# Optimization experiments

Hardware: AMD Instinct MI355X
Metric: run time of the kernel (lower is better)

## Reference

```python
import jax, jax.numpy as jnp
import numpy as np

H = 128          # input hidden dim
HID = 128        # expert hidden width
OUT = 128        # out_channels
NR = 8           # n_routed
NS = 2           # n_shared
RDIM = 16        # router feature dim


def setup_inputs() -> dict:
    key = jax.random.key(0)
    ks = jax.random.split(key, 11)
    s = 0.05
    x = jax.random.normal(ks[0], (2, 32, 32, 32, H), dtype=jnp.float32)
    # router params
    Wr1 = jax.random.normal(ks[1], (H, RDIM), dtype=jnp.float32) * s
    br1 = jnp.zeros((RDIM,), dtype=jnp.float32)
    Wr2 = jax.random.normal(ks[2], (RDIM, NR), dtype=jnp.float32) * s
    br2 = jnp.zeros((NR,), dtype=jnp.float32)
    # routed expert params, stacked on leading expert axis
    We1 = jax.random.normal(ks[3], (NR, H, HID), dtype=jnp.float32) * s
    be1 = jnp.zeros((NR, HID), dtype=jnp.float32)
    We2 = jax.random.normal(ks[4], (NR, HID, OUT), dtype=jnp.float32) * s
    be2 = jnp.zeros((NR, OUT), dtype=jnp.float32)
    # shared expert params
    Ws1 = jax.random.normal(ks[5], (NS, H, HID), dtype=jnp.float32) * s
    bs1 = jnp.zeros((NS, HID), dtype=jnp.float32)
    Ws2 = jax.random.normal(ks[6], (NS, HID, OUT), dtype=jnp.float32) * s
    bs2 = jnp.zeros((NS, OUT), dtype=jnp.float32)
    return dict(x=x, Wr1=Wr1, br1=br1, Wr2=Wr2, br2=br2,
                We1=We1, be1=be1, We2=We2, be2=be2,
                Ws1=Ws1, bs1=bs1, Ws2=Ws2, bs2=bs2)


def reference(x, Wr1, br1, Wr2, br2, We1, be1, We2, be2, Ws1, bs1, Ws2, bs2):
    # router: Dense(16) -> relu -> Dense(n_routed) -> softmax
    rf = jax.nn.relu(jnp.einsum('...h,hr->...r', x, Wr1) + br1)
    logits = jnp.einsum('...r,re->...e', rf, Wr2) + br2
    gate = jax.nn.softmax(logits, axis=-1)                      # [..., NR]
    threshold = 1.0 / NR
    mask = (gate > threshold).astype(gate.dtype)
    mg = gate * mask
    mg = mg / (jnp.sum(mg, axis=-1, keepdims=True) + 1e-8)
    # routed experts (batched over expert axis e): Dense -> gelu(tanh) -> Dense
    hr = jax.nn.gelu(jnp.einsum('...h,ehd->...ed', x, We1) + be1)   # [..., NR, HID]
    ro = jnp.einsum('...ed,edo->...eo', hr, We2) + be2              # [..., NR, OUT]
    routed_agg = jnp.einsum('...eo,...e->...o', ro, mg)
    # shared experts summed
    hs = jax.nn.gelu(jnp.einsum('...h,ehd->...ed', x, Ws1) + bs1)   # [..., NS, HID]
    so = jnp.einsum('...ed,edo->...eo', hs, Ws2) + bs2              # [..., NS, OUT]
    shared_agg = jnp.sum(so, axis=-2)
    return routed_agg + shared_agg
```

## Files before the change

### kernel.cpp

```cpp
#include <hip/hip_runtime.h>
#include <hip/hip_bf16.h>

typedef __bf16 bf16x8 __attribute__((ext_vector_type(8)));
typedef float  f32x16 __attribute__((ext_vector_type(16)));
typedef float  f32x4  __attribute__((ext_vector_type(4)));
typedef float  f32x2  __attribute__((ext_vector_type(2)));

static __device__ __forceinline__ f32x16 mfma32(bf16x8 a, bf16x8 b, f32x16 c) {
    return __builtin_amdgcn_mfma_f32_32x32x16_bf16(a, b, c, 0, 0, 0);
}

#define GELU_C1 2.30220820f
#define GELU_C2 0.10294324f

__global__ __launch_bounds__(256) void pack_kernel(
    const float* __restrict__ We1, const float* __restrict__ be1,
    const float* __restrict__ Ws1, const float* __restrict__ bs1,
    const float* __restrict__ We2, const float* __restrict__ Ws2,
    const float* __restrict__ Wr1, const float* __restrict__ br1,
    const float* __restrict__ Wr2, const float* __restrict__ br2,
    __bf16* __restrict__ w1p, __bf16* __restrict__ w2p,
    double* __restrict__ wr1d, double* __restrict__ br1d,
    double* __restrict__ wr2d, double* __restrict__ br2d)
{
    int tid = blockIdx.x * 256 + threadIdx.x;
    if (tid < 23040) {
        int l  = tid & 63;
        int ks = (tid >> 6) % 9;
        int nt = (tid / 576) & 3;
        int e  = tid / 2304;
        const float* src = (e < 8) ? (We1 + e * 16384) : (Ws1 + (e - 8) * 16384);
        const float* bia = (e < 8) ? (be1 + e * 128)   : (bs1 + (e - 8) * 128);
        int n = nt * 32 + (l & 31);
        int kb = ks * 16 + (l >> 5) * 8;
        bf16x8 v;
        #pragma unroll
        for (int j = 0; j < 8; ++j) {
            int k = kb + j;
            float f = (k < 128) ? src[k * 128 + n] : ((k == 128) ? bia[n] : 0.f);
            v[j] = (__bf16)f;
        }
        *(bf16x8*)(w1p + (size_t)tid * 8) = v;
    } else if (tid < 43520) {
        int t2 = tid - 23040;
        int l  = t2 & 63;
        int ks = (t2 >> 6) & 7;
        int ot = (t2 / 512) & 3;
        int e  = t2 / 2048;
        const float* src = (e < 8) ? (We2 + e * 16384) : (Ws2 + (e - 8) * 16384);
        int o  = ot * 32 + (l & 31);
        int lh = l >> 5;
        bf16x8 v;
        #pragma unroll
        for (int j = 0; j < 8; ++j) {
            int hid = 16 * ks + 8 * (j >> 2) + 4 * lh + (j & 3);
            v[j] = (__bf16)src[hid * 128 + o];
        }
        *(bf16x8*)(w2p + (size_t)t2 * 8) = v;
    } else if (tid < 45568) {
        int i = tid - 43520;
        wr1d[i] = (double)Wr1[i];
    } else if (tid < 45696) {
        int i = tid - 45568;
        wr2d[i] = (double)Wr2[i];
    } else if (tid < 45712) {
        int i = tid - 45696;
        br1d[i] = (double)br1[i];
    } else if (tid < 45720) {
        int i = tid - 45712;
        br2d[i] = (double)br2[i];
    }
}

__global__ __launch_bounds__(256, 2) void moe_main_kernel(
    const float* __restrict__ x,
    const double* __restrict__ wr1d, const double* __restrict__ br1d,
    const double* __restrict__ wr2d, const double* __restrict__ br2d,
    const __bf16* __restrict__ w1p, const __bf16* __restrict__ w2p,
    const float* __restrict__ be2, const float* __restrict__ bs2,
    float* __restrict__ out)
{
    __shared__ __align__(16) char lds[61952];
    float*  xs  = (float*)lds;
    __bf16* Xp  = (__bf16*)(lds + 33280);
    double* rfs = (double*)(lds + 51712);
    float*  mgs = (float*)(lds + 59904);
    float*  Red = (float*)lds;

    const int t    = threadIdx.x;
    const int lane = t & 63;
    const int wave = t >> 6;
    const int l31  = lane & 31;
    const int lh   = lane >> 5;
    const int mt   = wave >> 1;
    const int h    = wave & 1;
    const int tok0 = blockIdx.x * 64;

    #pragma unroll
    for (int i = 0; i < 4; ++i) {
        int g = i * 256 + t;
        int m = g >> 4;
        int c = g & 15;
        const f32x4* sp = (const f32x4*)(x + (size_t)(tok0 + m) * 128 + c * 8);
        f32x4 va = sp[0], vb = sp[1];
        float* xd = xs + m * 130 + c * 8;
        f32x2 s0, s1, s2, s3;
        s0[0]=va[0]; s0[1]=va[1]; s1[0]=va[2]; s1[1]=va[3];
        s2[0]=vb[0]; s2[1]=vb[1]; s3[0]=vb[2]; s3[1]=vb[3];
        *(f32x2*)(xd)     = s0; *(f32x2*)(xd + 2) = s1;
        *(f32x2*)(xd + 4) = s2; *(f32x2*)(xd + 6) = s3;
        bf16x8 v;
        v[0]=(__bf16)va[0]; v[1]=(__bf16)va[1]; v[2]=(__bf16)va[2]; v[3]=(__bf16)va[3];
        v[4]=(__bf16)vb[0]; v[5]=(__bf16)vb[1]; v[6]=(__bf16)vb[2]; v[7]=(__bf16)vb[3];
        *(bf16x8*)&Xp[(((m >> 5) * 9 + (c >> 1)) * 64 + (c & 1) * 32 + (m & 31)) * 8] = v;
    }
    if (t < 128) {
        int mtx = t >> 6, l = t & 63;
        bf16x8 v;
        #pragma unroll
        for (int j = 0; j < 8; ++j) v[j] = (__bf16)0.f;
        if (l < 32) v[0] = (__bf16)1.0f;
        *(bf16x8*)&Xp[((mtx * 9 + 8) * 64 + l) * 8] = v;
    }
    __syncthreads();

    {
        const int tok = t & 63;
        const int rq  = (t >> 6) * 4;
        const int rqs = __builtin_amdgcn_readfirstlane(rq);
        double rf4[4];
        #pragma unroll
        for (int j = 0; j < 4; ++j) rf4[j] = br1d[rqs + j];
        const float* xr = xs + tok * 130;
        #pragma unroll 4
        for (int c = 0; c < 64; ++c) {
            f32x2 xv2 = *(const f32x2*)(xr + c * 2);
            #pragma unroll
            for (int q = 0; q < 2; ++q) {
                double xv = (double)xv2[q];
                int k = c * 2 + q;
                #pragma unroll
                for (int j = 0; j < 4; ++j)
                    rf4[j] = fma(xv, wr1d[k * 16 + rqs + j], rf4[j]);
            }
        }
        #pragma unroll
        for (int j = 0; j < 4; ++j)
            rfs[tok * 16 + rq + j] = rf4[j] > 0.0 ? rf4[j] : 0.0;
    }
    __syncthreads();

    if (t < 64) {
        double lg[8];
        #pragma unroll
        for (int j = 0; j < 8; ++j) lg[j] = br2d[j];
        #pragma unroll
        for (int r = 0; r < 16; ++r) {
            double rv = rfs[t * 16 + r];
            #pragma unroll
            for (int j = 0; j < 8; ++j)
                lg[j] = fma(rv, wr2d[r * 8 + j], lg[j]);
        }
        double mx = lg[0];
        #pragma unroll
        for (int j = 1; j < 8; ++j) mx = lg[j] > mx ? lg[j] : mx;
        double ex[8]; double s = 0.0;
        #pragma unroll
        for (int j = 0; j < 8; ++j) { ex[j] = exp(lg[j] - mx); s += ex[j]; }
        double ms = 0.0;
        bool mk[8];
        #pragma unroll
        for (int j = 0; j < 8; ++j) {
            mk[j] = (8.0 * ex[j] > s);
            ms += mk[j] ? ex[j] : 0.0;
        }
        double inv = 1.0 / (ms + s * 1e-8);
        #pragma unroll
        for (int j = 0; j < 8; ++j)
            mgs[t * 8 + j] = mk[j] ? (float)(ex[j] * inv) : 0.f;
    }
    __syncthreads();

    const float* mgr = mgs + (32 * mt + l31) * 8;
    f32x4 ga4 = *(const f32x4*)mgr;
    f32x4 gb4 = *(const f32x4*)(mgr + 4);
    float gte[8] = {ga4[0], ga4[1], ga4[2], ga4[3], gb4[0], gb4[1], gb4[2], gb4[3]};

    f32x16 acc[4];
    #pragma unroll
    for (int ot = 0; ot < 4; ++ot)
        #pragma unroll
        for (int i = 0; i < 16; ++i) acc[ot][i] = 0.f;

    const bf16x8* w1v = (const bf16x8*)w1p;
    const bf16x8* w2v = (const bf16x8*)w2p;

    bf16x8 wbuf[2][9];
    {
        const bf16x8* p = w1v + ((size_t)(2 * h) * 9) * 64 + lane;
        #pragma unroll
        for (int ks = 0; ks < 9; ++ks) wbuf[0][ks] = p[ks * 64];
    }

    #pragma unroll 1
    for (int e = 0; e < 10; ++e) {
        const float gv = (e < 8) ? gte[e] : 1.0f;
        #pragma unroll
        for (int n2 = 0; n2 < 2; ++n2) {
            const bf16x8* wBp = w2v + ((size_t)(e * 4) * 8 + 4 * h + 2 * n2) * 64 + lane;
            bf16x8 wBc[8];
            #pragma unroll
            for (int ot = 0; ot < 4; ++ot)
                #pragma unroll
                for (int b = 0; b < 2; ++b)
                    wBc[ot * 2 + b] = wBp[(ot * 8 + b) * 64];

            f32x16 a1;
            #pragma unroll
            for (int i = 0; i < 16; ++i) a1[i] = 0.f;
            #pragma unroll
            for (int ks = 0; ks < 9; ++ks) {
                bf16x8 xb = *(const bf16x8*)&Xp[((mt * 9 + ks) * 64 + lane) * 8];
                a1 = mfma32(wbuf[n2][ks], xb, a1);
            }

            {
                int en  = (n2 == 0) ? e : (e < 9 ? e + 1 : 9);
                int ntn = (n2 == 0) ? (2 * h + 1) : (2 * h);
                const bf16x8* p = w1v + ((size_t)(en * 4 + ntn) * 9) * 64 + lane;
                #pragma unroll
                for (int ks = 0; ks < 9; ++ks) wbuf[n2 ^ 1][ks] = p[ks * 64];
            }

            #pragma unroll
            for (int b = 0; b < 2; ++b) {
                bf16x8 fr;
                #pragma unroll
                for (int jp = 0; jp < 4; ++jp) {
                    f32x2 hh; hh[0] = a1[8 * b + 2 * jp]; hh[1] = a1[8 * b + 2 * jp + 1];
                    f32x2 tt = hh * hh;
                    f32x2 pp;
                    pp[0] = fmaf(tt[0], -GELU_C2, -GELU_C1);
                    pp[1] = fmaf(tt[1], -GELU_C2, -GELU_C1);
                    f32x2 mm = hh * pp;
                    float e0 = __builtin_amdgcn_exp2f(mm[0]);
                    float e1 = __builtin_amdgcn_exp2f(mm[1]);
                    float q0 = __builtin_amdgcn_rcpf(1.f + e0);
                    float q1 = __builtin_amdgcn_rcpf(1.f + e1);
                    f32x2 gg; gg[0] = hh[0] * q0 * gv; gg[1] = hh[1] * q1 * gv;
                    fr[2 * jp]     = (__bf16)gg[0];
                    fr[2 * jp + 1] = (__bf16)gg[1];
                }
                acc[0] = mfma32(fr, wBc[0 * 2 + b], acc[0]);
                acc[1] = mfma32(fr, wBc[1 * 2 + b], acc[1]);
                acc[2] = mfma32(fr, wBc[2 * 2 + b], acc[2]);
                acc[3] = mfma32(fr, wBc[3 * 2 + b], acc[3]);
            }
        }
    }

    __syncthreads();
    if (h == 1) {
        #pragma unroll
        for (int ot = 0; ot < 4; ++ot)
            #pragma unroll
            for (int r = 0; r < 16; ++r)
                Red[((mt * 4 + ot) * 16 + r) * 64 + lane] = acc[ot][r];
    }
    __syncthreads();
    if (h == 0) {
        float be2c[4][8], bsc[4];
        #pragma unroll
        for (int ot = 0; ot < 4; ++ot) {
            int o = 32 * ot + l31;
            bsc[ot] = bs2[o] + bs2[128 + o];
            #pragma unroll
            for (int ee = 0; ee < 8; ++ee) be2c[ot][ee] = be2[ee * 128 + o];
        }
        const float* mgb = mgs + (32 * mt) * 8;
        #pragma unroll
        for (int r = 0; r < 16; ++r) {
            int mrow = (r & 3) + 8 * (r >> 2) + 4 * lh;
            f32x4 g0 = *(const f32x4*)&mgb[mrow * 8];
            f32x4 g1 = *(const f32x4*)&mgb[mrow * 8 + 4];
            size_t orow = (size_t)(tok0 + 32 * mt + mrow) * 128;
            #pragma unroll
            for (int ot = 0; ot < 4; ++ot) {
                float b = bsc[ot];
                #pragma unroll
                for (int ee = 0; ee < 4; ++ee) b = fmaf(g0[ee], be2c[ot][ee], b);
                #pragma unroll
                for (int ee = 0; ee < 4; ++ee) b = fmaf(g1[ee], be2c[ot][4 + ee], b);
                float v = acc[ot][r] + Red[((mt * 4 + ot) * 16 + r) * 64 + lane] + b;
                out[orow + 32 * ot + l31] = v;
            }
        }
    }
}

extern "C" void kernel_launch(void* const* d_in, const int* in_sizes, int n_in,
                              void* d_out, int out_size, void* d_ws, size_t ws_size,
                              hipStream_t stream)
{
    const float* x   = (const float*)d_in[0];
    const float* Wr1 = (const float*)d_in[1];
    const float* br1 = (const float*)d_in[2];
    const float* Wr2 = (const float*)d_in[3];
    const float* br2 = (const float*)d_in[4];
    const float* We1 = (const float*)d_in[5];
    const float* be1 = (const float*)d_in[6];
    const float* We2 = (const float*)d_in[7];
    const float* be2 = (const float*)d_in[8];
    const float* Ws1 = (const float*)d_in[9];
    const float* bs1 = (const float*)d_in[10];
    const float* Ws2 = (const float*)d_in[11];
    const float* bs2 = (const float*)d_in[12];

    __bf16* w1p  = (__bf16*)d_ws;
    __bf16* w2p  = (__bf16*)((char*)d_ws + 368640);
    double* wr1d = (double*)((char*)d_ws + 696320);
    double* wr2d = (double*)((char*)d_ws + 712704);
    double* br1d = (double*)((char*)d_ws + 713728);
    double* br2d = (double*)((char*)d_ws + 713856);

    pack_kernel<<<179, 256, 0, stream>>>(We1, be1, Ws1, bs1, We2, Ws2,
                                         Wr1, br1, Wr2, br2,
                                         w1p, w2p, wr1d, br1d, wr2d, br2d);
    moe_main_kernel<<<1024, 256, 0, stream>>>(x, wr1d, br1d, wr2d, br2d,
                                              w1p, w2p, be2, bs2, (float*)d_out);
}
```

Measured before the change: 176.5 us.

## Split router into separate kernel and share GELU hidden tile via LDS

Moves the fp64 router and gating into its own kernel that writes per-token gates to workspace, so the main kernel no longer holds fp32 x or fp64 router scratch in shared memory. The main MoE kernel now has each wave compute half the hidden columns, stage the gated GELU activations in LDS, and then compute half the output columns over the full hidden dimension. This removes the end-of-kernel cross-wave reduction, halves the accumulator registers, and raises the occupancy hint from 2 to 4 blocks. In exchange it reads x twice across two launches, adds two barriers per expert, and drops the double-buffered W1 prefetch.

```diff
diff --git a/kernel.cpp b/kernel.cpp
--- a/kernel.cpp
+++ b/kernel.cpp
@@ -2,6 +2,7 @@
 #include <hip/hip_bf16.h>
 
 typedef __bf16 bf16x8 __attribute__((ext_vector_type(8)));
+typedef __bf16 bf16x4 __attribute__((ext_vector_type(4)));
 typedef float  f32x16 __attribute__((ext_vector_type(16)));
 typedef float  f32x4  __attribute__((ext_vector_type(4)));
 typedef float  f32x2  __attribute__((ext_vector_type(2)));
@@ -72,28 +73,111 @@
     }
 }
 
-__global__ __launch_bounds__(256, 2) void moe_main_kernel(
+__global__ __launch_bounds__(256) void router_kernel(
     const float* __restrict__ x,
     const double* __restrict__ wr1d, const double* __restrict__ br1d,
     const double* __restrict__ wr2d, const double* __restrict__ br2d,
+    float* __restrict__ gates)
+{
+    __shared__ __align__(16) char lds[41472];
+    float*  xs  = (float*)lds;
+    double* rfs = (double*)(lds + 33280);
+
+    const int t    = threadIdx.x;
+    const int tok0 = blockIdx.x * 64;
+
+    #pragma unroll
+    for (int i = 0; i < 8; ++i) {
+        int cid = i * 256 + t;
+        int m = cid >> 5;
+        int c = cid & 31;
+        f32x4 v = *(const f32x4*)(x + (size_t)(tok0 + m) * 128 + c * 4);
+        f32x2 s0, s1;
+        s0[0] = v[0]; s0[1] = v[1]; s1[0] = v[2]; s1[1] = v[3];
+        *(f32x2*)(xs + m * 130 + c * 4)     = s0;
+        *(f32x2*)(xs + m * 130 + c * 4 + 2) = s1;
+    }
+    __syncthreads();
+
+    {
+        const int tok = t & 63;
+        const int rq  = (t >> 6) * 4;
+        const int rqs = __builtin_amdgcn_readfirstlane(rq);
+        double rf4[4];
+        #pragma unroll
+        for (int j = 0; j < 4; ++j) rf4[j] = br1d[rqs + j];
+        const float* xr = xs + tok * 130;
+        #pragma unroll 4
+        for (int c = 0; c < 64; ++c) {
+            f32x2 xv2 = *(const f32x2*)(xr + c * 2);
+            #pragma unroll
+            for (int q = 0; q < 2; ++q) {
+                double xv = (double)xv2[q];
+                int k = c * 2 + q;
+                #pragma unroll
+                for (int j = 0; j < 4; ++j)
+                    rf4[j] = fma(xv, wr1d[k * 16 + rqs + j], rf4[j]);
+            }
+        }
+        #pragma unroll
+        for (int j = 0; j < 4; ++j)
+            rfs[tok * 16 + rq + j] = rf4[j] > 0.0 ? rf4[j] : 0.0;
+    }
+    __syncthreads();
+
+    if (t < 64) {
+        double lg[8];
+        #pragma unroll
+        for (int j = 0; j < 8; ++j) lg[j] = br2d[j];
+        #pragma unroll
+        for (int r = 0; r < 16; ++r) {
+            double rv = rfs[t * 16 + r];
+            #pragma unroll
+            for (int j = 0; j < 8; ++j)
+                lg[j] = fma(rv, wr2d[r * 8 + j], lg[j]);
+        }
+        double mx = lg[0];
+        #pragma unroll
+        for (int j = 1; j < 8; ++j) mx = lg[j] > mx ? lg[j] : mx;
+        double ex[8]; double s = 0.0;
+        #pragma unroll
+        for (int j = 0; j < 8; ++j) { ex[j] = exp(lg[j] - mx); s += ex[j]; }
+        double ms = 0.0;
+        bool mk[8];
+        #pragma unroll
+        for (int j = 0; j < 8; ++j) {
+            mk[j] = (8.0 * ex[j] > s);
+            ms += mk[j] ? ex[j] : 0.0;
+        }
+        double inv = 1.0 / (ms + s * 1e-8);
+        f32x4 o0, o1;
+        #pragma unroll
+        for (int j = 0; j < 4; ++j) {
+            o0[j] = mk[j]     ? (float)(ex[j] * inv)     : 0.f;
+            o1[j] = mk[4 + j] ? (float)(ex[4 + j] * inv) : 0.f;
+        }
+        *(f32x4*)(gates + (size_t)(tok0 + t) * 8)     = o0;
+        *(f32x4*)(gates + (size_t)(tok0 + t) * 8 + 4) = o1;
+    }
+}
+
+__global__ __launch_bounds__(256, 4) void moe_main_kernel(
+    const float* __restrict__ x, const float* __restrict__ gates,
     const __bf16* __restrict__ w1p, const __bf16* __restrict__ w2p,
     const float* __restrict__ be2, const float* __restrict__ bs2,
     float* __restrict__ out)
 {
-    __shared__ __align__(16) char lds[61952];
-    float*  xs  = (float*)lds;
-    __bf16* Xp  = (__bf16*)(lds + 33280);
-    double* rfs = (double*)(lds + 51712);
-    float*  mgs = (float*)(lds + 59904);
-    float*  Red = (float*)lds;
+    __shared__ __align__(16) char lds[34816];
+    __bf16* Xp = (__bf16*)lds;
+    __bf16* Hs = (__bf16*)(lds + 18432);
 
     const int t    = threadIdx.x;
     const int lane = t & 63;
     const int wave = t >> 6;
     const int l31  = lane & 31;
-    const int lh   = lane >> 5;
+    const int hi   = lane >> 5;
     const int mt   = wave >> 1;
-    const int h    = wave & 1;
+    const int oh   = wave & 1;
     const int tok0 = blockIdx.x * 64;
 
     #pragma unroll
@@ -103,12 +187,6 @@
         int c = g & 15;
         const f32x4* sp = (const f32x4*)(x + (size_t)(tok0 + m) * 128 + c * 8);
         f32x4 va = sp[0], vb = sp[1];
-        float* xd = xs + m * 130 + c * 8;
-        f32x2 s0, s1, s2, s3;
-        s0[0]=va[0]; s0[1]=va[1]; s1[0]=va[2]; s1[1]=va[3];
-        s2[0]=vb[0]; s2[1]=vb[1]; s3[0]=vb[2]; s3[1]=vb[3];
-        *(f32x2*)(xd)     = s0; *(f32x2*)(xd + 2) = s1;
-        *(f32x2*)(xd + 4) = s2; *(f32x2*)(xd + 6) = s3;
         bf16x8 v;
         v[0]=(__bf16)va[0]; v[1]=(__bf16)va[1]; v[2]=(__bf16)va[2]; v[3]=(__bf16)va[3];
         v[4]=(__bf16)vb[0]; v[5]=(__bf16)vb[1]; v[6]=(__bf16)vb[2]; v[7]=(__bf16)vb[3];
@@ -124,176 +202,104 @@
     }
     __syncthreads();
 
-    {
-        const int tok = t & 63;
-        const int rq  = (t >> 6) * 4;
-        const int rqs = __builtin_amdgcn_readfirstlane(rq);
-        double rf4[4];
-        #pragma unroll
-        for (int j = 0; j < 4; ++j) rf4[j] = br1d[rqs + j];
-        const float* xr = xs + tok * 130;
-        #pragma unroll 4
-        for (int c = 0; c < 64; ++c) {
-            f32x2 xv2 = *(const f32x2*)(xr + c * 2);
-            #pragma unroll
-            for (int q = 0; q < 2; ++q) {
-                double xv = (double)xv2[q];
-                int k = c * 2 + q;
-                #pragma unroll
-                for (int j = 0; j < 4; ++j)
-                    rf4[j] = fma(xv, wr1d[k * 16 + rqs + j], rf4[j]);
-            }
-        }
-        #pragma unroll
-        for (int j = 0; j < 4; ++j)
-            rfs[tok * 16 + rq + j] = rf4[j] > 0.0 ? rf4[j] : 0.0;
-    }
-    __syncthreads();
-
-    if (t < 64) {
-        double lg[8];
-        #pragma unroll
-        for (int j = 0; j < 8; ++j) lg[j] = br2d[j];
-        #pragma unroll
-        for (int r = 0; r < 16; ++r) {
-            double rv = rfs[t * 16 + r];
-            #pragma unroll
-            for (int j = 0; j < 8; ++j)
-                lg[j] = fma(rv, wr2d[r * 8 + j], lg[j]);
-        }
-        double mx = lg[0];
-        #pragma unroll
-        for (int j = 1; j < 8; ++j) mx = lg[j] > mx ? lg[j] : mx;
-        double ex[8]; double s = 0.0;
-        #pragma unroll
-        for (int j = 0; j < 8; ++j) { ex[j] = exp(lg[j] - mx); s += ex[j]; }
-        double ms = 0.0;
-        bool mk[8];
-        #pragma unroll
-        for (int j = 0; j < 8; ++j) {
-            mk[j] = (8.0 * ex[j] > s);
-            ms += mk[j] ? ex[j] : 0.0;
-        }
-        double inv = 1.0 / (ms + s * 1e-8);
-        #pragma unroll
-        for (int j = 0; j < 8; ++j)
-            mgs[t * 8 + j] = mk[j] ? (float)(ex[j] * inv) : 0.f;
-    }
-    __syncthreads();
-
-    const float* mgr = mgs + (32 * mt + l31) * 8;
-    f32x4 ga4 = *(const f32x4*)mgr;
-    f32x4 gb4 = *(const f32x4*)(mgr + 4);
+    const float* gtp = gates + (size_t)(tok0 + 32 * mt + l31) * 8;
+    f32x4 ga4 = *(const f32x4*)gtp;
+    f32x4 gb4 = *(const f32x4*)(gtp + 4);
     float gte[8] = {ga4[0], ga4[1], ga4[2], ga4[3], gb4[0], gb4[1], gb4[2], gb4[3]};
 
-    f32x16 acc[4];
+    f32x16 acc0, acc1;
     #pragma unroll
-    for (int ot = 0; ot < 4; ++ot)
-        #pragma unroll
-        for (int i = 0; i < 16; ++i) acc[ot][i] = 0.f;
+    for (int i = 0; i < 16; ++i) { acc0[i] = 0.f; acc1[i] = 0.f; }
 
     const bf16x8* w1v = (const bf16x8*)w1p;
     const bf16x8* w2v = (const bf16x8*)w2p;
-
-    bf16x8 wbuf[2][9];
-    {
-        const bf16x8* p = w1v + ((size_t)(2 * h) * 9) * 64 + lane;
-        #pragma unroll
-        for (int ks = 0; ks < 9; ++ks) wbuf[0][ks] = p[ks * 64];
-    }
 
     #pragma unroll 1
     for (int e = 0; e < 10; ++e) {
         const float gv = (e < 8) ? gte[e] : 1.0f;
-        #pragma unroll
-        for (int n2 = 0; n2 < 2; ++n2) {
-            const bf16x8* wBp = w2v + ((size_t)(e * 4) * 8 + 4 * h + 2 * n2) * 64 + lane;
-            bf16x8 wBc[8];
-            #pragma unroll
-            for (int ot = 0; ot < 4; ++ot)
-                #pragma unroll
-                for (int b = 0; b < 2; ++b)
-                    wBc[ot * 2 + b] = wBp[(ot * 8 + b) * 64];
-
+
+        #pragma unroll
+        for (int nti = 0; nti < 2; ++nti) {
+            const int nt = 2 * oh + nti;
+            const bf16x8* wp = w1v + ((size_t)(e * 4 + nt) * 9) * 64 + lane;
+            bf16x8 wb[9];
+            #pragma unroll
+            for (int ks = 0; ks < 9; ++ks) wb[ks] = wp[ks * 64];
             f32x16 a1;
             #pragma unroll
             for (int i = 0; i < 16; ++i) a1[i] = 0.f;
             #pragma unroll
             for (int ks = 0; ks < 9; ++ks) {
                 bf16x8 xb = *(const bf16x8*)&Xp[((mt * 9 + ks) * 64 + lane) * 8];
-                a1 = mfma32(wbuf[n2][ks], xb, a1);
-            }
-
-            {
-                int en  = (n2 == 0) ? e : (e < 9 ? e + 1 : 9);
-                int ntn = (n2 == 0) ? (2 * h + 1) : (2 * h);
-                const bf16x8* p = w1v + ((size_t)(en * 4 + ntn) * 9) * 64 + lane;
+                a1 = mfma32(wb[ks], xb, a1);
+            }
+            #pragma unroll
+            for (int g4 = 0; g4 < 4; ++g4) {
+                bf16x4 pk;
                 #pragma unroll
-                for (int ks = 0; ks < 9; ++ks) wbuf[n2 ^ 1][ks] = p[ks * 64];
-            }
-
-            #pragma unroll
-            for (int b = 0; b < 2; ++b) {
-                bf16x8 fr;
-                #pragma unroll
-                for (int jp = 0; jp < 4; ++jp) {
-                    f32x2 hh; hh[0] = a1[8 * b + 2 * jp]; hh[1] = a1[8 * b + 2 * jp + 1];
-                    f32x2 tt = hh * hh;
-                    f32x2 pp;
-                    pp[0] = fmaf(tt[0], -GELU_C2, -GELU_C1);
-                    pp[1] = fmaf(tt[1], -GELU_C2, -GELU_C1);
-                    f32x2 mm = hh * pp;
-                    float e0 = __builtin_amdgcn_exp2f(mm[0]);
-                    float e1 = __builtin_amdgcn_exp2f(mm[1]);
+                for (int qp = 0; qp < 2; ++qp) {
+                    float h0 = a1[4 * g4 + 2 * qp];
+                    float h1 = a1[4 * g4 + 2 * qp + 1];
+                    float t0 = h0 * h0, t1 = h1 * h1;
+                    float p0 = fmaf(t0, -GELU_C2, -GELU_C1);
+                    float p1 = fmaf(t1, -GELU_C2, -GELU_C1);
+                    float m0 = h0 * p0, m1 = h1 * p1;
+                    float e0 = __builtin_amdgcn_exp2f(m0);
+                    float e1 = __builtin_amdgcn_exp2f(m1);
                     float q0 = __builtin_amdgcn_rcpf(1.f + e0);
                     float q1 = __builtin_amdgcn_rcpf(1.f + e1);
-                    f32x2 gg; gg[0] = hh[0] * q0 * gv; gg[1] = hh[1] * q1 * gv;
-                    fr[2 * jp]     = (__bf16)gg[0];
-                    fr[2 * jp + 1] = (__bf16)gg[1];
+                    pk[2 * qp]     = (__bf16)(h0 * q0 * gv);
+                    pk[2 * qp + 1] = (__bf16)(h1 * q1 * gv);
                 }
-                acc[0] = mfma32(fr, wBc[0 * 2 + b], acc[0]);
-                acc[1] = mfma32(fr, wBc[1 * 2 + b], acc[1]);
-                acc[2] = mfma32(fr, wBc[2 * 2 + b], acc[2]);
-                acc[3] = mfma32(fr, wBc[3 * 2 + b], acc[3]);
-            }
-        }
-    }
-
-    __syncthreads();
-    if (h == 1) {
-        #pragma unroll
-        for (int ot = 0; ot < 4; ++ot)
-            #pragma unroll
-            for (int r = 0; r < 16; ++r)
-                Red[((mt * 4 + ot) * 16 + r) * 64 + lane] = acc[ot][r];
-    }
-    __syncthreads();
-    if (h == 0) {
-        float be2c[4][8], bsc[4];
-        #pragma unroll
-        for (int ot = 0; ot < 4; ++ot) {
-            int o = 32 * ot + l31;
-            bsc[ot] = bs2[o] + bs2[128 + o];
-            #pragma unroll
-            for (int ee = 0; ee < 8; ++ee) be2c[ot][ee] = be2[ee * 128 + o];
-        }
-        const float* mgb = mgs + (32 * mt) * 8;
+                *(bf16x4*)&Hs[((mt * 8 + 2 * nt + (g4 >> 1)) * 64 + lane) * 8
+                              + 4 * (g4 & 1)] = pk;
+            }
+        }
+        __syncthreads();
+
+        {
+            const bf16x8* wBp = w2v + ((size_t)e * 32 + (2 * oh) * 8) * 64 + lane;
+            #pragma unroll
+            for (int kq = 0; kq < 8; ++kq) {
+                bf16x8 hf = *(const bf16x8*)&Hs[((mt * 8 + kq) * 64 + lane) * 8];
+                bf16x8 wB0 = wBp[kq * 64];
+                bf16x8 wB1 = wBp[(8 + kq) * 64];
+                acc0 = mfma32(hf, wB0, acc0);
+                acc1 = mfma32(hf, wB1, acc1);
+            }
+        }
+        __syncthreads();
+    }
+
+    {
+        float be2c[2][8], bsc[2];
+        #pragma unroll
+        for (int oti = 0; oti < 2; ++oti) {
+            int o = 32 * (2 * oh + oti) + l31;
+            bsc[oti] = bs2[o] + bs2[128 + o];
+            #pragma unroll
+            for (int ee = 0; ee < 8; ++ee) be2c[oti][ee] = be2[ee * 128 + o];
+        }
+        const float* mgb = gates + (size_t)(tok0 + 32 * mt) * 8;
         #pragma unroll
         for (int r = 0; r < 16; ++r) {
-            int mrow = (r & 3) + 8 * (r >> 2) + 4 * lh;
+            int mrow = (r & 3) + 8 * (r >> 2) + 4 * hi;
             f32x4 g0 = *(const f32x4*)&mgb[mrow * 8];
             f32x4 g1 = *(const f32x4*)&mgb[mrow * 8 + 4];
             size_t orow = (size_t)(tok0 + 32 * mt + mrow) * 128;
-            #pragma unroll
-            for (int ot = 0; ot < 4; ++ot) {
-                float b = bsc[ot];
-                #pragma unroll
-                for (int ee = 0; ee < 4; ++ee) b = fmaf(g0[ee], be2c[ot][ee], b);
-                #pragma unroll
-                for (int ee = 0; ee < 4; ++ee) b = fmaf(g1[ee], be2c[ot][4 + ee], b);
-                float v = acc[ot][r] + Red[((mt * 4 + ot) * 16 + r) * 64 + lane] + b;
-                out[orow + 32 * ot + l31] = v;
-            }
+            float b0 = bsc[0], b1 = bsc[1];
+            #pragma unroll
+            for (int ee = 0; ee < 4; ++ee) {
+                b0 = fmaf(g0[ee], be2c[0][ee], b0);
+                b1 = fmaf(g0[ee], be2c[1][ee], b1);
+            }
+            #pragma unroll
+            for (int ee = 0; ee < 4; ++ee) {
+                b0 = fmaf(g1[ee], be2c[0][4 + ee], b0);
+                b1 = fmaf(g1[ee], be2c[1][4 + ee], b1);
+            }
+            out[orow + 32 * (2 * oh)     + l31] = acc0[r] + b0;
+            out[orow + 32 * (2 * oh + 1) + l31] = acc1[r] + b1;
         }
     }
 }
@@ -322,10 +328,12 @@
     double* wr2d = (double*)((char*)d_ws + 712704);
     double* br1d = (double*)((char*)d_ws + 713728);
     double* br2d = (double*)((char*)d_ws + 713856);
+    float*  gts  = (float*)((char*)d_ws + 720896);
 
     pack_kernel<<<179, 256, 0, stream>>>(We1, be1, Ws1, bs1, We2, Ws2,
                                          Wr1, br1, Wr2, br2,
                                          w1p, w2p, wr1d, br1d, wr2d, br2d);
-    moe_main_kernel<<<1024, 256, 0, stream>>>(x, wr1d, br1d, wr2d, br2d,
-                                              w1p, w2p, be2, bs2, (float*)d_out);
-}
+    router_kernel<<<1024, 256, 0, stream>>>(x, wr1d, br1d, wr2d, br2d, gts);
+    moe_main_kernel<<<1024, 256, 0, stream>>>(x, gts, w1p, w2p, be2, bs2,
+                                              (float*)d_out);
+}
```

After: 184.8 us. +4.7%, slower.
